# Optimization experiments

Measured on AMD Instinct MI355X. Metric: run time of the kernel, lower is better.

## Reference

```python
import jax, jax.numpy as jnp
import numpy as np

B, T, D = 16, 4096, 1024
HID = 4 * D // 3  # 1365, per SelectorMLP(hidden=4*d//3)
RHO, TAU, LN_EPS = 0.2, 1.0, 1e-5


def setup_inputs() -> dict:
    key = jax.random.key(0)
    ks = jax.random.split(key, 6)
    embeddings = jax.random.normal(ks[0], (B, T, D), dtype=jnp.float32)
    attn = (jax.random.uniform(ks[1], (B, T)) < 0.9).astype(jnp.float32)
    ln_w = jnp.ones((D,), jnp.float32)
    ln_b = jnp.zeros((D,), jnp.float32)
    fc1_w = jax.random.normal(ks[2], (HID, D), jnp.float32) * (1.0 / np.sqrt(D))
    fc1_b = jnp.zeros((HID,), jnp.float32)
    fc2_w = jax.random.normal(ks[3], (1, HID), jnp.float32) * (1.0 / np.sqrt(HID))
    fc2_b = jnp.zeros((1,), jnp.float32)
    return {"embeddings": embeddings, "attn": attn, "ln_w": ln_w, "ln_b": ln_b,
            "fc1_w": fc1_w, "fc1_b": fc1_b, "fc2_w": fc2_w, "fc2_b": fc2_b}


def _hard_topk(z, K):
    # z: [B,T], K: [B,1] float integer budgets -> exact top-K 0/1 mask per row
    b, t = z.shape
    order = jnp.argsort(-z, axis=1)                       # descending sort indices
    mask = (jnp.arange(t)[None, :] < K).astype(z.dtype)   # [B,T] first-K ranks
    h = jnp.zeros_like(z).at[jnp.arange(b)[:, None], order].set(mask)
    return h


def reference(embeddings, attn, ln_w, ln_b, fc1_w, fc1_b, fc2_w, fc2_b):
    emb = embeddings * attn[:, :, None]                    # [B,T,D]
    # SelectorMLP (dropout = identity in eval)
    mu = jnp.mean(emb, axis=-1, keepdims=True)
    var = jnp.mean(jnp.square(emb - mu), axis=-1, keepdims=True)
    x = (emb - mu) / jnp.sqrt(var + LN_EPS) * ln_w + ln_b
    x = jax.nn.gelu(jnp.einsum('btd,hd->bth', x, fc1_w) + fc1_b, approximate=False)
    scores = jnp.einsum('bth,oh->bto', x, fc2_w)[..., 0] + fc2_b[0]  # [B,T]
    scores = jnp.where(attn == 0, -1e9, scores)
    p = jax.nn.softmax(scores / TAU, axis=1)
    entropy = -jnp.sum(p * jnp.log(p + 1e-12), axis=1)     # [B]
    T_eff = jnp.clip(jnp.sum(attn, axis=1), 1, None)
    norm_entropy = jnp.mean(entropy / jnp.log(T_eff))
    T_eff2 = jnp.sum(attn, axis=1, keepdims=True)          # [B,1]
    K = jnp.clip(jnp.round(RHO * T_eff2), 1, None)
    z = K * p
    h = _hard_topk(z, K)
    g = h + (z - jax.lax.stop_gradient(z))                 # straight-through
    return g, z, norm_entropy
```

## Files before the change

### kernel.cpp

```cpp
#include <hip/hip_runtime.h>
#include <math.h>

#define B_ 16
#define T_ 4096
#define D_ 1024
#define HID_ 1365
#define NPAD 1408
#define NGRP 88
#define N_TOK (B_*T_)
#define RHO_ 0.2f
#define LN_EPS_ 1e-5f
#define SC 1024.0f
#define INV_SC2 (1.0f/(1024.0f*1024.0f))

#define NHT 11
#define WCHUNKS (NGRP*32*4*16)
#define NG16 4096
#define ACHUNKS ((size_t)NG16*32*64)

typedef _Float16 f16x8 __attribute__((ext_vector_type(8)));
typedef float f32x4 __attribute__((ext_vector_type(4)));

__device__ __forceinline__ void gl16(const void* g, void* l) {
  __builtin_amdgcn_global_load_lds(
      (const __attribute__((address_space(1))) unsigned int*)g,
      (__attribute__((address_space(3))) unsigned int*)l, 16, 0, 0);
}

__global__ __launch_bounds__(256) void wsplit_kernel(
    const float* __restrict__ fc1w, f16x8* __restrict__ whi, f16x8* __restrict__ wlo)
{
  int c = blockIdx.x * 256 + threadIdx.x;
  if (c >= WCHUNKS) return;
  int ln = c & 15, q = (c >> 4) & 3, ks = (c >> 6) & 31, g = c >> 11;
  int n = g * 16 + ln;
  int k = ks * 32 + q * 8;
  f16x8 hi, lo;
#pragma unroll
  for (int j = 0; j < 8; ++j) {
    float v = (n < HID_) ? fc1w[(size_t)n * D_ + k + j] * SC : 0.f;
    _Float16 h = (_Float16)v;
    hi[j] = h;
    lo[j] = (_Float16)(v - (float)h);
  }
  whi[c] = hi;
  wlo[c] = lo;
}

#define FSTR 1028
__global__ __launch_bounds__(256, 2) void lnasplit_kernel(
    const float* __restrict__ emb, const float* __restrict__ attn,
    const float* __restrict__ lnw, const float* __restrict__ lnb,
    f16x8* __restrict__ ahi, f16x8* __restrict__ alo)
{
  __shared__ float tile[16 * FSTR];
  __shared__ float smu[16], srs[16];
  int tid = threadIdx.x;
  int g = blockIdx.x;
  int wave = tid >> 6, lane = tid & 63;
#pragma unroll
  for (int it = 0; it < 16; ++it) {
    int idx = tid + it * 256;
    int row = idx >> 8, c4 = idx & 255;
    float a = attn[g * 16 + row];
    float4 v = *reinterpret_cast<const float4*>(
        emb + (size_t)(g * 16 + row) * D_ + c4 * 4);
    v.x *= a; v.y *= a; v.z *= a; v.w *= a;
    *reinterpret_cast<float4*>(&tile[row * FSTR + c4 * 4]) = v;
  }
  __syncthreads();
#pragma unroll
  for (int r4 = 0; r4 < 4; ++r4) {
    int row = wave * 4 + r4;
    float s = 0.f, sq = 0.f;
#pragma unroll
    for (int q = 0; q < 4; ++q) {
      float4 v = *reinterpret_cast<const float4*>(&tile[row * FSTR + lane * 4 + q * 256]);
      s  += v.x + v.y + v.z + v.w;
      sq += v.x * v.x + v.y * v.y + v.z * v.z + v.w * v.w;
    }
#pragma unroll
    for (int off = 32; off > 0; off >>= 1) {
      s  += __shfl_down(s, off, 64);
      sq += __shfl_down(sq, off, 64);
    }
    if (lane == 0) {
      float m = s * (1.f / D_);
      float var = sq * (1.f / D_) - m * m;
      if (var < 0.f) var = 0.f;
      smu[row] = m;
      srs[row] = 1.f / sqrtf(var + LN_EPS_);
    }
  }
  __syncthreads();
#pragma unroll
  for (int it = 0; it < 8; ++it) {
    int idx = tid + it * 256;
    int ksl = idx >> 6, l = idx & 63;
    int ln = l & 15, q = l >> 4;
    float rs = srs[ln];
    float nmr = -smu[ln] * rs;
    int colbase = ksl * 32 + q * 8;
    float4 e0 = *reinterpret_cast<const float4*>(&tile[ln * FSTR + colbase]);
    float4 e1 = *reinterpret_cast<const float4*>(&tile[ln * FSTR + colbase + 4]);
    float ev[8] = {e0.x, e0.y, e0.z, e0.w, e1.x, e1.y, e1.z, e1.w};
    f16x8 hi, lo;
#pragma unroll
    for (int j = 0; j < 8; ++j) {
      int kg = colbase + j;
      float wv = lnw[kg], bv = lnb[kg];
      float y = fmaf(ev[j] * rs, wv, fmaf(nmr, wv, bv)) * SC;
      _Float16 h = (_Float16)y;
      hi[j] = h;
      lo[j] = (_Float16)(y - (float)h);
    }
    size_t c = (size_t)(g * 32 + ksl) * 64 + l;
    ahi[c] = hi;
    alo[c] = lo;
  }
}

__global__ __launch_bounds__(256, 2) void mfma_score_v5(
    const f16x8* __restrict__ ahi, const f16x8* __restrict__ alo,
    const f16x8* __restrict__ whi, const f16x8* __restrict__ wlo,
    const float* __restrict__ fc1b, const float* __restrict__ fc2w,
    float* __restrict__ partial)
{
  __shared__ f16x8 sbuf[2][2048];
  __shared__ float red[2][128];
  int tid = threadIdx.x, lane = tid & 63;
  int w = tid >> 6, wrow = w & 1, wcol = w >> 1;
  int flat = blockIdx.x;
  int xcd = flat & 7, j = flat >> 3;
  int tb = xcd * 64 + j / NHT;
  int ht = j % NHT;
  int g0 = tb * 8;
  int hb0 = ht * 8;
  int ln16 = lane & 15, quad = lane >> 4;

  const f16x8* src = (w == 0) ? ahi : (w == 1) ? alo : (w == 2) ? whi : wlo;
  size_t grpbase = (w < 2) ? (size_t)g0 : (size_t)hb0;
  const f16x8* sp = src + grpbase * 32 * 64 + lane;

  auto STAGE = [&](int buf, int ks) {
#pragma unroll
    for (int i = 0; i < 8; ++i)
      gl16(sp + (size_t)(i * 32 + ks) * 64, &sbuf[buf][w * 512 + i * 64]);
  };

  STAGE(0, 0);

  f32x4 acc[4][4];
#pragma unroll
  for (int i = 0; i < 4; ++i)
#pragma unroll
    for (int j2 = 0; j2 < 4; ++j2) acc[i][j2] = (f32x4)0.f;

  __syncthreads();

#pragma unroll 2
  for (int ks = 0; ks < 32; ++ks) {
    int cur = ks & 1;
    if (ks < 31) STAGE(cur ^ 1, ks + 1);
    f16x8 ah[4], al[4], bh[4], bl[4];
#pragma unroll
    for (int mi = 0; mi < 4; ++mi) {
      ah[mi] = sbuf[cur][(wrow * 4 + mi) * 64 + lane];
      al[mi] = sbuf[cur][512 + (wrow * 4 + mi) * 64 + lane];
    }
#pragma unroll
    for (int nj = 0; nj < 4; ++nj) {
      bh[nj] = sbuf[cur][1024 + (wcol * 4 + nj) * 64 + lane];
      bl[nj] = sbuf[cur][1536 + (wcol * 4 + nj) * 64 + lane];
    }
#pragma unroll
    for (int mi = 0; mi < 4; ++mi)
#pragma unroll
      for (int nj = 0; nj < 4; ++nj) {
        acc[mi][nj] = __builtin_amdgcn_mfma_f32_16x16x32_f16(ah[mi], bh[nj], acc[mi][nj], 0, 0, 0);
        acc[mi][nj] = __builtin_amdgcn_mfma_f32_16x16x32_f16(al[mi], bh[nj], acc[mi][nj], 0, 0, 0);
        acc[mi][nj] = __builtin_amdgcn_mfma_f32_16x16x32_f16(ah[mi], bl[nj], acc[mi][nj], 0, 0, 0);
      }
    __syncthreads();
  }

  int gb0 = hb0 + wcol * 4;
  float s[4][4];
#pragma unroll
  for (int mi = 0; mi < 4; ++mi)
#pragma unroll
    for (int r = 0; r < 4; ++r) s[mi][r] = 0.f;
#pragma unroll
  for (int nj = 0; nj < 4; ++nj) {
    int h = (gb0 + nj) * 16 + ln16;
    float b1 = 0.f, w2 = 0.f;
    if (h < HID_) { b1 = fc1b[h]; w2 = fc2w[h]; }
#pragma unroll
    for (int mi = 0; mi < 4; ++mi)
#pragma unroll
      for (int r = 0; r < 4; ++r) {
        float v = acc[mi][nj][r] * INV_SC2 + b1;
        float gel = 0.5f * v * (1.f + erff(v * 0.70710678118654752440f));
        s[mi][r] = fmaf(gel, w2, s[mi][r]);
      }
  }
#pragma unroll
  for (int mi = 0; mi < 4; ++mi)
#pragma unroll
    for (int r = 0; r < 4; ++r) {
      float v = s[mi][r];
      v += __shfl_xor(v, 1, 64);
      v += __shfl_xor(v, 2, 64);
      v += __shfl_xor(v, 4, 64);
      v += __shfl_xor(v, 8, 64);
      s[mi][r] = v;
    }
  if (ln16 == 0) {
#pragma unroll
    for (int mi = 0; mi < 4; ++mi)
#pragma unroll
      for (int r = 0; r < 4; ++r)
        red[wcol][wrow * 64 + mi * 16 + quad * 4 + r] = s[mi][r];
  }
  __syncthreads();
  if (tid < 128)
    partial[(size_t)ht * N_TOK + tb * 128 + tid] = red[0][tid] + red[1][tid];
}

__global__ __launch_bounds__(1024) void softmax_kernel(
    const float* __restrict__ partial, const float* __restrict__ fc2b,
    const float* __restrict__ attn,
    float* __restrict__ out_z, float* __restrict__ rowent, float* __restrict__ rowK)
{
  __shared__ float buf[1024];
  int b = blockIdx.x, tid = threadIdx.x;
  const float* arow = attn + b * T_;
  float sv[4], av[4];
  float f2b = fc2b[0];
#pragma unroll
  for (int q = 0; q < 4; ++q) {
    int t = tid + q * 1024;
    av[q] = arow[t];
    float sc = f2b;
#pragma unroll
    for (int p = 0; p < NHT; ++p) sc += partial[(size_t)p * N_TOK + b * T_ + t];
    sv[q] = (av[q] == 0.f) ? -1e9f : sc;
  }
  float m = fmaxf(fmaxf(sv[0], sv[1]), fmaxf(sv[2], sv[3]));
  buf[tid] = m; __syncthreads();
  for (int s = 512; s > 0; s >>= 1) { if (tid < s) buf[tid] = fmaxf(buf[tid], buf[tid + s]); __syncthreads(); }
  m = buf[0]; __syncthreads();
  float e[4]; float es = 0.f, as = 0.f;
#pragma unroll
  for (int q = 0; q < 4; ++q) { e[q] = expf(sv[q] - m); es += e[q]; as += av[q]; }
  buf[tid] = es; __syncthreads();
  for (int s = 512; s > 0; s >>= 1) { if (tid < s) buf[tid] += buf[tid + s]; __syncthreads(); }
  es = buf[0]; __syncthreads();
  buf[tid] = as; __syncthreads();
  for (int s = 512; s > 0; s >>= 1) { if (tid < s) buf[tid] += buf[tid + s]; __syncthreads(); }
  as = buf[0]; __syncthreads();
  float K = fmaxf(1.f, rintf(RHO_ * as));
  float inv = 1.f / es;
  float ent = 0.f;
#pragma unroll
  for (int q = 0; q < 4; ++q) {
    float p = e[q] * inv;
    out_z[b * T_ + tid + q * 1024] = K * p;
    ent -= p * logf(p + 1e-12f);
  }
  buf[tid] = ent; __syncthreads();
  for (int s = 512; s > 0; s >>= 1) { if (tid < s) buf[tid] += buf[tid + s]; __syncthreads(); }
  if (tid == 0) {
    rowent[b] = buf[0] / logf(fmaxf(as, 1.f));
    rowK[b] = K;
  }
}

__global__ __launch_bounds__(1024) void topk_kernel(
    const float* __restrict__ zall, float* __restrict__ g,
    const float* __restrict__ rowent, const float* __restrict__ rowK,
    float* __restrict__ out_scalar)
{
  __shared__ float sm[T_];
  __shared__ int s_first, s_last;
  int b = blockIdx.x, tid = threadIdx.x;
  const float* zrow = zall + b * T_;
  for (int t = tid; t < T_; t += 1024) sm[t] = zrow[t];
  __syncthreads();
  for (int k = 2; k <= T_; k <<= 1) {
    for (int j = k >> 1; j > 0; j >>= 1) {
      for (int t = tid; t < T_; t += 1024) {
        int ixj = t ^ j;
        if (ixj > t) {
          float a = sm[t], c = sm[ixj];
          bool desc = ((t & k) == 0);
          if (desc ? (a < c) : (a > c)) { sm[t] = c; sm[ixj] = a; }
        }
      }
      __syncthreads();
    }
  }
  int K = (int)rowK[b];
  float thr = sm[K - 1];
  if (tid == 0) { s_first = T_; s_last = -1; }
  __syncthreads();
  for (int t = tid; t < T_; t += 1024) {
    if (sm[t] == thr) { atomicMin(&s_first, t); atomicMax(&s_last, t); }
  }
  __syncthreads();
  int cgt = s_first;
  int eqTotal = s_last - s_first + 1;
  int need = K - cgt;
  float* grow = g + b * T_;
  bool allEq = (eqTotal == need);
  for (int t = tid; t < T_; t += 1024) {
    float zv = zrow[t];
    if (zv > thr) grow[t] = 1.f;
    else if (zv < thr) grow[t] = 0.f;
    else if (allEq) grow[t] = 1.f;
  }
  __syncthreads();
  if (!allEq && tid == 0) {
    int cnt = 0;
    for (int t = 0; t < T_; ++t) {
      float zv = zrow[t];
      if (zv == thr) { grow[t] = (cnt < need) ? 1.f : 0.f; ++cnt; }
    }
  }
  if (b == 0 && tid == 0) {
    float s = 0.f;
    for (int i = 0; i < B_; ++i) s += rowent[i];
    out_scalar[0] = s * (1.f / B_);
  }
}

extern "C" void kernel_launch(void* const* d_in, const int* in_sizes, int n_in,
                              void* d_out, int out_size, void* d_ws, size_t ws_size,
                              hipStream_t stream)
{
  const float* emb  = (const float*)d_in[0];
  const float* attn = (const float*)d_in[1];
  const float* lnw  = (const float*)d_in[2];
  const float* lnb  = (const float*)d_in[3];
  const float* fc1w = (const float*)d_in[4];
  const float* fc1b = (const float*)d_in[5];
  const float* fc2w = (const float*)d_in[6];
  const float* fc2b = (const float*)d_in[7];

  float* out = (float*)d_out;
  float* g  = out;
  float* z  = out + N_TOK;
  float* ns = out + 2 * N_TOK;

  float* mu      = (float*)d_ws;
  float* rstd    = mu + N_TOK;
  float* partial = rstd + N_TOK;
  float* rowent  = partial + (size_t)NHT * N_TOK;
  float* rowK    = rowent + 16;
  f16x8* whi     = (f16x8*)(rowK + 16);
  f16x8* wlo     = whi + WCHUNKS;
  f16x8* ahi     = wlo + WCHUNKS;
  f16x8* alo     = ahi + ACHUNKS;

  wsplit_kernel<<<(WCHUNKS + 255) / 256, 256, 0, stream>>>(fc1w, whi, wlo);
  lnasplit_kernel<<<NG16, 256, 0, stream>>>(emb, attn, lnw, lnb, ahi, alo);
  mfma_score_v5<<<8 * 64 * NHT, 256, 0, stream>>>(ahi, alo, whi, wlo, fc1b, fc2w, partial);
  softmax_kernel<<<B_, 1024, 0, stream>>>(partial, fc2b, attn, z, rowent, rowK);
  topk_kernel<<<B_, 1024, 0, stream>>>(z, g, rowent, rowK, ns);
}
```

Measured before the change: 1.080 ms.

## Enlarge score GEMM tile to 256 tokens with triple-buffered LDS pipeline

The MFMA score kernel moves to 512 threads (8 waves in a 4x2 layout) covering 256 tokens per block instead of 128. This halves how often the weight tiles are reloaded per token. LDS staging goes from double to triple buffering, with two stages in flight, explicit vmcnt waits and raw s_barrier in place of __syncthreads. MFMA sections are raised with s_setprio to favour matrix issue over the loads. LDS use rises to about 144KB per block, which may limit residency to one block per CU despite launch_bounds(512,2), and the grid shrinks by half.

```diff
diff --git a/kernel.cpp b/kernel.cpp
--- a/kernel.cpp
+++ b/kernel.cpp
@@ -120,35 +120,71 @@
   }
 }
 
-__global__ __launch_bounds__(256, 2) void mfma_score_v5(
+__global__ __launch_bounds__(512, 2) void mfma_score_v6(
     const f16x8* __restrict__ ahi, const f16x8* __restrict__ alo,
     const f16x8* __restrict__ whi, const f16x8* __restrict__ wlo,
     const float* __restrict__ fc1b, const float* __restrict__ fc2w,
     float* __restrict__ partial)
 {
-  __shared__ f16x8 sbuf[2][2048];
-  __shared__ float red[2][128];
+  __shared__ f16x8 sbuf[3][3072];
+  __shared__ float red[2][256];
   int tid = threadIdx.x, lane = tid & 63;
-  int w = tid >> 6, wrow = w & 1, wcol = w >> 1;
+  int w = tid >> 6, wrow = w & 3, wcol = w >> 2;
   int flat = blockIdx.x;
   int xcd = flat & 7, j = flat >> 3;
-  int tb = xcd * 64 + j / NHT;
+  int tb = xcd * 32 + j / NHT;
   int ht = j % NHT;
-  int g0 = tb * 8;
+  int g0 = tb * 16;
   int hb0 = ht * 8;
   int ln16 = lane & 15, quad = lane >> 4;
 
-  const f16x8* src = (w == 0) ? ahi : (w == 1) ? alo : (w == 2) ? whi : wlo;
-  size_t grpbase = (w < 2) ? (size_t)g0 : (size_t)hb0;
-  const f16x8* sp = src + grpbase * 32 * 64 + lane;
-
-  auto STAGE = [&](int buf, int ks) {
-#pragma unroll
-    for (int i = 0; i < 8; ++i)
-      gl16(sp + (size_t)(i * 32 + ks) * 64, &sbuf[buf][w * 512 + i * 64]);
-  };
-
-  STAGE(0, 0);
+  int u0 = w * 6;
+  const f16x8* sp[6];
+#pragma unroll
+  for (int i = 0; i < 6; ++i) {
+    int u = u0 + i;
+    const f16x8* base;
+    int grp;
+    if (u < 16)      { base = ahi; grp = g0 + u; }
+    else if (u < 32) { base = alo; grp = g0 + (u - 16); }
+    else if (u < 40) { base = whi; grp = hb0 + (u - 32); }
+    else             { base = wlo; grp = hb0 + (u - 40); }
+    sp[i] = base + (size_t)grp * 2048 + lane;
+  }
+
+#define STAGE6(BUF, KS)                                                \
+  _Pragma("unroll")                                                    \
+  for (int i = 0; i < 6; ++i)                                          \
+    gl16(sp[i] + (size_t)(KS) * 64, &sbuf[BUF][(u0 + i) * 64]);
+
+#define DOSTEP(KS, CUR, STG, VMSTR)                                    \
+  {                                                                    \
+    if (STG) { STAGE6(((CUR) + 2) % 3, (KS) + 2); }                    \
+    f16x8 ah[4], al[4], bh[4], bl[4];                                  \
+    _Pragma("unroll")                                                  \
+    for (int mi = 0; mi < 4; ++mi) {                                   \
+      ah[mi] = sbuf[CUR][(wrow * 4 + mi) * 64 + lane];                 \
+      al[mi] = sbuf[CUR][1024 + (wrow * 4 + mi) * 64 + lane];          \
+    }                                                                  \
+    _Pragma("unroll")                                                  \
+    for (int nj = 0; nj < 4; ++nj) {                                   \
+      bh[nj] = sbuf[CUR][2048 + (wcol * 4 + nj) * 64 + lane];          \
+      bl[nj] = sbuf[CUR][2560 + (wcol * 4 + nj) * 64 + lane];          \
+    }                                                                  \
+    __builtin_amdgcn_s_setprio(1);                                     \
+    _Pragma("unroll")                                                  \
+    for (int mi = 0; mi < 4; ++mi)                                     \
+      _Pragma("unroll")                                                \
+      for (int nj = 0; nj < 4; ++nj) {                                 \
+        acc[mi][nj] = __builtin_amdgcn_mfma_f32_16x16x32_f16(ah[mi], bh[nj], acc[mi][nj], 0, 0, 0); \
+        acc[mi][nj] = __builtin_amdgcn_mfma_f32_16x16x32_f16(al[mi], bh[nj], acc[mi][nj], 0, 0, 0); \
+        acc[mi][nj] = __builtin_amdgcn_mfma_f32_16x16x32_f16(ah[mi], bl[nj], acc[mi][nj], 0, 0, 0); \
+      }                                                                \
+    __builtin_amdgcn_s_setprio(0);                                     \
+    __builtin_amdgcn_sched_barrier(0);                                 \
+    asm volatile("s_waitcnt " VMSTR ::: "memory");                     \
+    __builtin_amdgcn_s_barrier();                                      \
+  }
 
   f32x4 acc[4][4];
 #pragma unroll
@@ -156,33 +192,23 @@
 #pragma unroll
     for (int j2 = 0; j2 < 4; ++j2) acc[i][j2] = (f32x4)0.f;
 
-  __syncthreads();
-
-#pragma unroll 2
-  for (int ks = 0; ks < 32; ++ks) {
-    int cur = ks & 1;
-    if (ks < 31) STAGE(cur ^ 1, ks + 1);
-    f16x8 ah[4], al[4], bh[4], bl[4];
-#pragma unroll
-    for (int mi = 0; mi < 4; ++mi) {
-      ah[mi] = sbuf[cur][(wrow * 4 + mi) * 64 + lane];
-      al[mi] = sbuf[cur][512 + (wrow * 4 + mi) * 64 + lane];
-    }
-#pragma unroll
-    for (int nj = 0; nj < 4; ++nj) {
-      bh[nj] = sbuf[cur][1024 + (wcol * 4 + nj) * 64 + lane];
-      bl[nj] = sbuf[cur][1536 + (wcol * 4 + nj) * 64 + lane];
-    }
-#pragma unroll
-    for (int mi = 0; mi < 4; ++mi)
-#pragma unroll
-      for (int nj = 0; nj < 4; ++nj) {
-        acc[mi][nj] = __builtin_amdgcn_mfma_f32_16x16x32_f16(ah[mi], bh[nj], acc[mi][nj], 0, 0, 0);
-        acc[mi][nj] = __builtin_amdgcn_mfma_f32_16x16x32_f16(al[mi], bh[nj], acc[mi][nj], 0, 0, 0);
-        acc[mi][nj] = __builtin_amdgcn_mfma_f32_16x16x32_f16(ah[mi], bl[nj], acc[mi][nj], 0, 0, 0);
-      }
-    __syncthreads();
-  }
+  STAGE6(0, 0);
+  STAGE6(1, 1);
+  __builtin_amdgcn_sched_barrier(0);
+  asm volatile("s_waitcnt vmcnt(6)" ::: "memory");
+  __builtin_amdgcn_s_barrier();
+
+#pragma unroll 1
+  for (int kt = 0; kt < 30; kt += 3) {
+    DOSTEP(kt,     0, 1, "vmcnt(6)");
+    DOSTEP(kt + 1, 1, 1, "vmcnt(6)");
+    DOSTEP(kt + 2, 2, 1, "vmcnt(6)");
+  }
+  DOSTEP(30, 0, 0, "vmcnt(0)");
+  DOSTEP(31, 1, 0, "vmcnt(0)");
+
+#undef DOSTEP
+#undef STAGE6
 
   int gb0 = hb0 + wcol * 4;
   float s[4][4];
@@ -223,8 +249,8 @@
         red[wcol][wrow * 64 + mi * 16 + quad * 4 + r] = s[mi][r];
   }
   __syncthreads();
-  if (tid < 128)
-    partial[(size_t)ht * N_TOK + tb * 128 + tid] = red[0][tid] + red[1][tid];
+  if (tid < 256)
+    partial[(size_t)ht * N_TOK + tb * 256 + tid] = red[0][tid] + red[1][tid];
 }
 
 __global__ __launch_bounds__(1024) void softmax_kernel(
@@ -364,7 +390,7 @@
 
   wsplit_kernel<<<(WCHUNKS + 255) / 256, 256, 0, stream>>>(fc1w, whi, wlo);
   lnasplit_kernel<<<NG16, 256, 0, stream>>>(emb, attn, lnw, lnb, ahi, alo);
-  mfma_score_v5<<<8 * 64 * NHT, 256, 0, stream>>>(ahi, alo, whi, wlo, fc1b, fc2w, partial);
+  mfma_score_v6<<<8 * 32 * NHT, 512, 0, stream>>>(ahi, alo, whi, wlo, fc1b, fc2w, partial);
   softmax_kernel<<<B_, 1024, 0, stream>>>(partial, fc2b, attn, z, rowent, rowK);
   topk_kernel<<<B_, 1024, 0, stream>>>(z, g, rowent, rowK, ns);
 }
```

Result: slower. 1.186 ms (+9.7%).
